# Kernel tuning notes

Hardware: AMD Instinct MI355X
Metric: run time of the kernel (lower is better)

Reference implementation:

```python
import jax, jax.numpy as jnp
import numpy as np

B, S, D, FF, E, TOP_K = 4, 2048, 1024, 4096, 8, 2


def setup_inputs() -> dict:
    key = jax.random.key(0)
    ks = jax.random.split(key, 13)
    sd = 1.0 / np.sqrt(D)
    sf = 1.0 / np.sqrt(FF)
    return {
        "x":   jax.random.normal(ks[0], (B, S, D), jnp.float32),
        # parallel 2-way router
        "Wr":  jax.random.normal(ks[1], (D, 2), jnp.float32) * sd,
        "br":  jnp.zeros((2,), jnp.float32),
        # MoE gate
        "Wg":  jax.random.normal(ks[2], (D, E), jnp.float32) * sd,
        "bg":  jnp.zeros((E,), jnp.float32),
        # expert FFNs
        "W1":  jax.random.normal(ks[3], (E, D, FF), jnp.float32) * sd,
        "b1":  jnp.zeros((E, FF), jnp.float32),
        "W2":  jax.random.normal(ks[4], (E, FF, D), jnp.float32) * sf,
        "b2":  jnp.zeros((E, D), jnp.float32),
        # dense FFN
        "D1":  jax.random.normal(ks[5], (D, FF), jnp.float32) * sd,
        "d1b": jnp.zeros((FF,), jnp.float32),
        "D2":  jax.random.normal(ks[6], (FF, D), jnp.float32) * sf,
        "d2b": jnp.zeros((D,), jnp.float32),
    }


def _hybrid_moe(x, Wr, br, Wg, bg, W1, b1, W2, b2, D1, d1b, D2, d2b):
    b, s, d = x.shape
    t = x.reshape(-1, d)                                  # [T, D]
    T = t.shape[0]

    # parallel 2-way blend router
    rp = jax.nn.softmax(x @ Wr + br, axis=-1)             # [B, S, 2]

    # MoE gating: softmax over experts, top-k, renormalize
    gp = jax.nn.softmax(t @ Wg + bg, axis=-1)             # [T, E]
    vals, idx = jax.lax.top_k(gp, TOP_K)                  # [T, K]
    vals = vals / jnp.sum(vals, axis=-1, keepdims=True)
    cw = jnp.zeros((T, E), t.dtype).at[jnp.arange(T)[:, None], idx].add(vals)  # [T, E]

    # expert FFNs (ReLU MLP), combined with top-k weights
    h = jax.nn.relu(jnp.einsum('td,edf->tef', t, W1) + b1)       # [T, E, FF]
    eo = jnp.einsum('tef,efd->ted', h, W2) + b2                  # [T, E, D]
    moe = jnp.einsum('te,ted->td', cw, eo).reshape(b, s, d)

    # dense FFN branch
    dense = jax.nn.relu(x @ D1 + d1b) @ D2 + d2b

    return rp[..., 0:1] * moe + rp[..., 1:2] * dense


def reference(x, Wr, br, Wg, bg, W1, b1, W2, b2, D1, d1b, D2, d2b):
    return _hybrid_moe(x, Wr, br, Wg, bg, W1, b1, W2, b2, D1, d1b, D2, d2b)
```

## Files before the change

kernel.cpp:

```cpp
#include <hip/hip_runtime.h>
#include <stdint.h>

#define T_TOK   8192
#define D_DIM   1024
#define FF_DIM  4096
#define E_NUM   8
#define SLOT_MAX 18432
#define RT_MAX  104

typedef unsigned int   u32;
typedef unsigned short u16;
typedef __attribute__((ext_vector_type(4))) float  f32x4;
typedef __attribute__((ext_vector_type(4))) float  f4;
typedef __attribute__((ext_vector_type(8))) short  bf16x8;
typedef __attribute__((ext_vector_type(8))) unsigned short u16x8;

__device__ __forceinline__ u16 f2bf(float f) {
  u32 u = __builtin_bit_cast(u32, f);
  return (u16)((u + 0x7fffu + ((u >> 16) & 1u)) >> 16);
}
__device__ __forceinline__ float bf2f(u16 h) {
  u32 u = ((u32)h) << 16; return __builtin_bit_cast(float, u);
}

typedef const __attribute__((address_space(1))) u32* gp1_t;
typedef __attribute__((address_space(3))) u32*       lp3_t;
__device__ __forceinline__ void gload16(const u16* g, u16* l) {
  __builtin_amdgcn_global_load_lds((gp1_t)(const void*)g, (lp3_t)l, 16, 0, 0);
}

__global__ void k_init(int* hdr) { if (threadIdx.x < 64) hdr[threadIdx.x] = 0; }

__global__ __launch_bounds__(256) void k_route(
    const float* __restrict__ x, const float* __restrict__ Wr, const float* __restrict__ br,
    const float* __restrict__ Wg, const float* __restrict__ bg,
    int* __restrict__ hdr, int4* __restrict__ tok_sel, float4* __restrict__ tok_wf,
    u16* __restrict__ xb)
{
  int w = threadIdx.x >> 6, l = threadIdx.x & 63;
  int t = blockIdx.x * 4 + w;
  const float* xt = x + (size_t)t * D_DIM;
  u16* xbt = xb + (size_t)t * D_DIM;
  float p[10];
  #pragma unroll
  for (int i = 0; i < 10; ++i) p[i] = 0.f;
  for (int j = 0; j < D_DIM / 64; ++j) {
    int d = j * 64 + l;
    float xv = xt[d];
    xbt[d] = f2bf(xv);
    p[0] += xv * Wr[d * 2 + 0];
    p[1] += xv * Wr[d * 2 + 1];
    f4 g0 = *(const f4*)&Wg[d * 8];
    f4 g1 = *(const f4*)&Wg[d * 8 + 4];
    p[2] += xv * g0[0]; p[3] += xv * g0[1]; p[4] += xv * g0[2]; p[5] += xv * g0[3];
    p[6] += xv * g1[0]; p[7] += xv * g1[1]; p[8] += xv * g1[2]; p[9] += xv * g1[3];
  }
  #pragma unroll
  for (int off = 32; off; off >>= 1) {
    #pragma unroll
    for (int i = 0; i < 10; ++i) p[i] += __shfl_xor(p[i], off, 64);
  }
  if (l == 0) {
    float a0 = p[0] + br[0], a1 = p[1] + br[1];
    float m  = fmaxf(a0, a1);
    float e0 = __expf(a0 - m), e1 = __expf(a1 - m);
    float rs = 1.f / (e0 + e1);
    float rp0 = e0 * rs, rp1 = e1 * rs;
    float g[E_NUM]; float gm = -1e30f;
    #pragma unroll
    for (int e = 0; e < E_NUM; ++e) { g[e] = p[2 + e] + bg[e]; gm = fmaxf(gm, g[e]); }
    int i0 = 0;
    #pragma unroll
    for (int e = 1; e < E_NUM; ++e) if (g[e] > g[i0]) i0 = e;
    int i1 = (i0 == 0) ? 1 : 0;
    #pragma unroll
    for (int e = 0; e < E_NUM; ++e) if (e != i0 && g[e] > g[i1]) i1 = e;
    float x0 = __expf(g[i0] - gm), x1 = __expf(g[i1] - gm);
    float s = 1.f / (x0 + x1);
    int r0 = atomicAdd(&hdr[i0], 1);
    int r1 = atomicAdd(&hdr[i1], 1);
    tok_sel[t] = make_int4(i0, r0, i1, r1);
    tok_wf[t]  = make_float4(x0 * s, x1 * s, rp0, rp1);
  }
}

__global__ __launch_bounds__(256) void k_offsets(int* __restrict__ hdr,
                                                 int4* __restrict__ tilemap,
                                                 int* __restrict__ perm)
{
  __shared__ int soff[E_NUM + 1];
  int tid = threadIdx.x;
  if (tid == 0) {
    int acc = 0;
    for (int e = 0; e < E_NUM; ++e) {
      soff[e] = acc; hdr[8 + e] = acc;
      acc += (hdr[e] + 255) & ~255;
    }
    soff[E_NUM] = acc;
    hdr[16] = acc;
    hdr[17] = acc >> 8;
    hdr[18] = (acc >> 8) + T_TOK / 256;
  }
  __syncthreads();
  int nmoe = soff[E_NUM] >> 8;
  for (int rt = tid; rt < RT_MAX; rt += 256) {
    int4 ent;
    if (rt < nmoe) {
      int row0 = rt * 256;
      int e = 0;
      while (e < E_NUM - 1 && row0 >= soff[e + 1]) ++e;
      ent = make_int4(0, row0, e, 0);
    } else if (rt < nmoe + T_TOK / 256) {
      ent = make_int4(1, (rt - nmoe) * 256, -1, 0);
    } else {
      ent = make_int4(-1, 0, 0, 0);
    }
    tilemap[rt] = ent;
  }
  for (int s = tid; s < SLOT_MAX; s += 256) perm[s] = -1;
}

__global__ void k_scatter(const int4* __restrict__ tok_sel, const int* __restrict__ hdr,
                          int* __restrict__ perm, int2* __restrict__ tok_slot)
{
  int t = blockIdx.x * 256 + threadIdx.x;
  if (t >= T_TOK) return;
  int4 s = tok_sel[t];
  int s0 = hdr[8 + s.x] + s.y;
  int s1 = hdr[8 + s.z] + s.w;
  perm[s0] = t; perm[s1] = t;
  tok_slot[t] = make_int2(s0, s1);
}

__global__ __launch_bounds__(256) void k_gather(const u16* __restrict__ xb,
                                                const int* __restrict__ perm,
                                                const int* __restrict__ hdr,
                                                u16* __restrict__ xg)
{
  int nslots = hdr[16];
  int row = blockIdx.x * 2 + (threadIdx.x >> 7);
  if (row >= nslots) return;
  int lane = threadIdx.x & 127;
  int t = perm[row];
  u16x8* dst = (u16x8*)(xg + (size_t)row * D_DIM) + lane;
  if (t < 0) { u16x8 z = {0,0,0,0,0,0,0,0}; *dst = z; }
  else       { *dst = *((const u16x8*)(xb + (size_t)t * D_DIM) + lane); }
}

__global__ __launch_bounds__(256) void k_tcast_all(
    const float* __restrict__ W1, const float* __restrict__ W2,
    const float* __restrict__ D1, const float* __restrict__ D2,
    u16* __restrict__ W1bt, u16* __restrict__ W2bt,
    u16* __restrict__ D1bt, u16* __restrict__ D2bt)
{
  int bid = blockIdx.x;
  int panel = bid >> 10, pb = bid & 1023;
  const float* s; u16* d; int R, C, ltc;
  if (panel < 8)       { s = W1 + (size_t)panel * D_DIM * FF_DIM; d = W1bt + (size_t)panel * D_DIM * FF_DIM; R = D_DIM;  C = FF_DIM; ltc = 6; }
  else if (panel < 16) { int e = panel - 8;
                         s = W2 + (size_t)e * FF_DIM * D_DIM;     d = W2bt + (size_t)e * FF_DIM * D_DIM;     R = FF_DIM; C = D_DIM;  ltc = 4; }
  else if (panel == 16){ s = D1; d = D1bt; R = D_DIM;  C = FF_DIM; ltc = 6; }
  else                 { s = D2; d = D2bt; R = FF_DIM; C = D_DIM;  ltc = 4; }
  int tc = pb & ((1 << ltc) - 1), tr = pb >> ltc;

  __shared__ float tile[64][65];
  int t = threadIdx.x;
  #pragma unroll
  for (int p = 0; p < 4; ++p) {
    int r = p * 16 + (t >> 4);
    int c4 = (t & 15) * 4;
    f4 v = *(const f4*)&s[(size_t)(tr * 64 + r) * C + tc * 64 + c4];
    tile[r][c4+0] = v[0]; tile[r][c4+1] = v[1]; tile[r][c4+2] = v[2]; tile[r][c4+3] = v[3];
  }
  __syncthreads();
  #pragma unroll
  for (int q = 0; q < 2; ++q) {
    int oc = q * 32 + (t >> 3);
    int r8 = (t & 7) * 8;
    u16x8 o;
    #pragma unroll
    for (int j = 0; j < 8; ++j) o[j] = f2bf(tile[r8 + j][oc]);
    *(u16x8*)&d[(size_t)(tc * 64 + oc) * R + tr * 64 + r8] = o;
  }
}

#define LGKM0() { asm volatile("s_waitcnt lgkmcnt(0)" ::: "memory"); \
                  __builtin_amdgcn_sched_barrier(0); }
#define BAR()   __builtin_amdgcn_s_barrier()

template <int RELU>
__global__ __launch_bounds__(512, 2) void k_gemm8p(
    const u16* __restrict__ Amoe, const u16* __restrict__ Aden,
    const u16* __restrict__ Bexp, const u16* __restrict__ Bden,
    const float* __restrict__ biasexp, const float* __restrict__ biasden,
    u16* __restrict__ Omoe, u16* __restrict__ Oden,
    const int* __restrict__ hdr, const int4* __restrict__ tilemap,
    int K, int N, long bexp_stride, int biasexp_stride, int lg2gx)
{
  int gx  = 1 << lg2gx;
  int nwg = gx * gridDim.y;
  int lin = blockIdx.y * gx + blockIdx.x;
  int sw  = (lin & 7) * (nwg >> 3) + (lin >> 3);
  int ct  = sw & (gx - 1);
  int rt  = sw >> lg2gx;
  if (rt >= hdr[18]) return;

  int4 ent = tilemap[rt];
  const u16* A; const u16* B; const float* bias; u16* O;
  if (ent.x == 1) { A = Aden; B = Bden; bias = biasden; O = Oden; }
  else {
    A = Amoe; B = Bexp + (size_t)ent.z * bexp_stride;
    bias = biasexp + (size_t)ent.z * biasexp_stride;
    O = Omoe;
  }
  const int row0 = ent.y;

  __shared__ __align__(16) u16 lds[65536];

  const int tid = threadIdx.x;
  const int wid = tid >> 6, l = tid & 63;
  const int wm = wid >> 2, wn = wid & 3;

  const int skel = ((l & 7) ^ (l >> 3)) * 8;
  const u16* aStage = A + (size_t)(row0     + wid * 8 + (l >> 3)) * K + skel;
  const u16* bStage = B + (size_t)(ct * 256 + wid * 8 + (l >> 3)) * K + skel;

  const int fr = l & 15, fq = l >> 4;
  const int fx = (l & 7) << 4;
  const int cs0 = (fq * 16) ^ fx;
  const int cs1 = (64 + fq * 16) ^ fx;
  const int brow = (wn & 1) * 64;
  const char* ldsc = (const char*)lds;
  const char* aP0 = ldsc + wm * 16384 + fr * 128 + cs0;
  const char* aP1 = ldsc + wm * 16384 + fr * 128 + cs1;
  const char* bP0 = ldsc + 65536 + (wn >> 1) * 16384 + (brow + fr) * 128 + cs0;
  const char* bP1 = ldsc + 65536 + (wn >> 1) * 16384 + (brow + fr) * 128 + cs1;

  auto STAGE_A = [&](int tt, int h, int bb) {
    const u16* src = aStage + (size_t)(h * 128) * K + (size_t)tt * 64;
    u16* dst = &lds[(bb * 2 + h) * 8192 + wid * 512];
    gload16(src, dst);
    gload16(src + (size_t)64 * K, dst + 4096);
  };
  auto STAGE_B = [&](int tt, int h, int bb) {
    const u16* src = bStage + (size_t)(h * 128) * K + (size_t)tt * 64;
    u16* dst = &lds[32768 + (bb * 2 + h) * 8192 + wid * 512];
    gload16(src, dst);
    gload16(src + (size_t)64 * K, dst + 4096);
  };

  f32x4 acc[8][4];
  #pragma unroll
  for (int m = 0; m < 8; ++m)
    #pragma unroll
    for (int n = 0; n < 4; ++n) acc[m][n] = (f32x4){0.f, 0.f, 0.f, 0.f};

  bf16x8 a0[4][2], a1[4][2], b0[2][2], b1[2][2];

  #define READ_A0(B_) { _Pragma("unroll") for (int j = 0; j < 4; ++j) { \
      a0[j][0] = *(const bf16x8*)(aP0 + ((B_)*32768 + j*2048)); \
      a0[j][1] = *(const bf16x8*)(aP1 + ((B_)*32768 + j*2048)); } }
  #define READ_A1(B_) { _Pragma("unroll") for (int j = 0; j < 4; ++j) { \
      a1[j][0] = *(const bf16x8*)(aP0 + ((B_)*32768 + 8192 + j*2048)); \
      a1[j][1] = *(const bf16x8*)(aP1 + ((B_)*32768 + 8192 + j*2048)); } }
  #define READ_B0(B_) { _Pragma("unroll") for (int i = 0; i < 2; ++i) { \
      b0[i][0] = *(const bf16x8*)(bP0 + ((B_)*32768 + i*2048)); \
      b0[i][1] = *(const bf16x8*)(bP1 + ((B_)*32768 + i*2048)); } }
  #define READ_B1(B_) { _Pragma("unroll") for (int i = 0; i < 2; ++i) { \
      b1[i][0] = *(const bf16x8*)(bP0 + ((B_)*32768 + 4096 + i*2048)); \
      b1[i][1] = *(const bf16x8*)(bP1 + ((B_)*32768 + 4096 + i*2048)); } }
  #define MFMA_Q(am, bm, mo, no) { __builtin_amdgcn_s_setprio(1); \
    _Pragma("unroll") for (int j = 0; j < 4; ++j) \
      _Pragma("unroll") for (int i = 0; i < 2; ++i) { \
        acc[(mo) + j][(no) + i] = __builtin_amdgcn_mfma_f32_16x16x32_bf16(am[j][0], bm[i][0], acc[(mo) + j][(no) + i], 0, 0, 0); \
        acc[(mo) + j][(no) + i] = __builtin_amdgcn_mfma_f32_16x16x32_bf16(am[j][1], bm[i][1], acc[(mo) + j][(no) + i], 0, 0, 0); } \
    __builtin_amdgcn_s_setprio(0); }

  const int NK = K >> 6;

  STAGE_B(0, 0, 0); STAGE_B(0, 1, 0); STAGE_A(0, 0, 0); STAGE_A(0, 1, 0);
  STAGE_B(1, 0, 1); STAGE_B(1, 1, 1); STAGE_A(1, 0, 1);
  asm volatile("s_waitcnt vmcnt(6)" ::: "memory");
  BAR();

  #define TILE(B_, t_) { \
     \
    READ_A0(B_); READ_B0(B_); \
    if ((t_) + 1 < NK) STAGE_A((t_) + 1, 1, (B_) ^ 1); \
    BAR(); LGKM0(); \
    MFMA_Q(a0, b0, 0, 0); \
    BAR(); \
     \
    READ_B1(B_); \
    BAR(); LGKM0(); \
    MFMA_Q(a0, b1, 0, 2); \
    BAR(); \
     \
    READ_A1(B_); \
    if ((t_) + 2 < NK) STAGE_B((t_) + 2, 0, (B_)); \
    BAR(); LGKM0(); \
    MFMA_Q(a1, b1, 4, 2); \
    BAR(); \
     \
    if ((t_) + 2 < NK) { STAGE_B((t_) + 2, 1, (B_)); STAGE_A((t_) + 2, 0, (B_)); } \
    BAR(); \
    MFMA_Q(a1, b0, 4, 0); \
    if ((t_) < NK - 2) { asm volatile("s_waitcnt vmcnt(6)" ::: "memory"); } \
    else               { asm volatile("s_waitcnt vmcnt(0)" ::: "memory"); } \
    BAR(); \
    __builtin_amdgcn_sched_barrier(0); }

  for (int t = 0; t < NK; t += 2) {
    TILE(0, t);
    TILE(1, t + 1);
  }
  #undef TILE

  __syncthreads();
  float bv[4];
  #pragma unroll
  for (int ni = 0; ni < 4; ++ni) bv[ni] = bias[ct * 256 + wn * 64 + ni * 16 + fr];
  float* ep = (float*)((char*)lds + wid * 4608);
  const int row16 = l >> 2, cg = l & 3;
  #pragma unroll
  for (int mi = 0; mi < 8; ++mi) {
    #pragma unroll
    for (int ni = 0; ni < 4; ++ni) {
      f32x4 v = acc[mi][ni];
      #pragma unroll
      for (int j = 0; j < 4; ++j) {
        float f = v[j] + bv[ni];
        if (RELU) f = fmaxf(f, 0.f);
        ep[(fq * 4 + j) * 68 + ni * 16 + fr] = f;
      }
    }
    #pragma unroll
    for (int p = 0; p < 2; ++p) {
      f4 r0 = *(f4*)&ep[row16 * 68 + (cg + p * 4) * 8];
      f4 r1 = *(f4*)&ep[row16 * 68 + (cg + p * 4) * 8 + 4];
      u16x8 o;
      o[0]=f2bf(r0[0]); o[1]=f2bf(r0[1]); o[2]=f2bf(r0[2]); o[3]=f2bf(r0[3]);
      o[4]=f2bf(r1[0]); o[5]=f2bf(r1[1]); o[6]=f2bf(r1[2]); o[7]=f2bf(r1[3]);
      int rr = row0 + wm * 128 + mi * 16 + row16;
      int cc = ct * 256 + wn * 64 + (cg + p * 4) * 8;
      *(u16x8*)&O[(size_t)rr * N + cc] = o;
    }
  }
  #undef READ_A0
  #undef READ_A1
  #undef READ_B0
  #undef READ_B1
  #undef MFMA_Q
}

__global__ __launch_bounds__(128) void k_combine(
    const u16* __restrict__ eo, const u16* __restrict__ dense_o,
    const float4* __restrict__ tok_wf, const int2* __restrict__ tok_slot,
    float* __restrict__ out)
{
  int t = blockIdx.x;
  int c8 = threadIdx.x;
  float4 wf = tok_wf[t];
  int2 sl = tok_slot[t];
  u16x8 a  = *((const u16x8*)(eo + (size_t)sl.x * D_DIM) + c8);
  u16x8 b  = *((const u16x8*)(eo + (size_t)sl.y * D_DIM) + c8);
  u16x8 dn = *((const u16x8*)(dense_o + (size_t)t * D_DIM) + c8);
  float* op = out + (size_t)t * D_DIM + c8 * 8;
  #pragma unroll
  for (int j = 0; j < 8; ++j) {
    float mo = wf.x * bf2f(a[j]) + wf.y * bf2f(b[j]);
    op[j] = wf.z * mo + wf.w * bf2f(dn[j]);
  }
}

extern "C" void kernel_launch(void* const* d_in, const int* in_sizes, int n_in,
                              void* d_out, int out_size, void* d_ws, size_t ws_size,
                              hipStream_t stream)
{
  const float* x   = (const float*)d_in[0];
  const float* Wr  = (const float*)d_in[1];
  const float* br  = (const float*)d_in[2];
  const float* Wg  = (const float*)d_in[3];
  const float* bg  = (const float*)d_in[4];
  const float* W1  = (const float*)d_in[5];
  const float* b1  = (const float*)d_in[6];
  const float* W2  = (const float*)d_in[7];
  const float* b2  = (const float*)d_in[8];
  const float* D1  = (const float*)d_in[9];
  const float* d1b = (const float*)d_in[10];
  const float* D2  = (const float*)d_in[11];
  const float* d2b = (const float*)d_in[12];
  float* out = (float*)d_out;

  char* base = (char*)d_ws;
  size_t cur = 0;
  auto alloc = [&](size_t b) -> void* {
    void* p = base + cur; cur = (cur + b + 255) & ~(size_t)255; return p;
  };
  int*    hdr      = (int*)   alloc(256 * sizeof(int));
  int4*   tilemap  = (int4*)  alloc((size_t)RT_MAX * sizeof(int4));
  int4*   tok_sel  = (int4*)  alloc((size_t)T_TOK * sizeof(int4));
  float4* tok_wf   = (float4*)alloc((size_t)T_TOK * sizeof(float4));
  int2*   tok_slot = (int2*)  alloc((size_t)T_TOK * sizeof(int2));
  int*    perm     = (int*)   alloc((size_t)SLOT_MAX * sizeof(int));
  u16*    xb       = (u16*)   alloc((size_t)T_TOK * D_DIM * 2);
  u16*    xg       = (u16*)   alloc((size_t)SLOT_MAX * D_DIM * 2);
  u16*    W1bt     = (u16*)   alloc((size_t)E_NUM * D_DIM * FF_DIM * 2);
  u16*    W2bt     = (u16*)   alloc((size_t)E_NUM * D_DIM * FF_DIM * 2);
  u16*    D1bt     = (u16*)   alloc((size_t)D_DIM * FF_DIM * 2);
  u16*    D2bt     = (u16*)   alloc((size_t)D_DIM * FF_DIM * 2);
  u16*    h_moe    = (u16*)   alloc((size_t)SLOT_MAX * FF_DIM * 2);
  u16*    h_dense  = (u16*)   alloc((size_t)T_TOK * FF_DIM * 2);
  u16*    eo       = (u16*)   alloc((size_t)SLOT_MAX * D_DIM * 2);
  u16*    dense_o  = (u16*)   alloc((size_t)T_TOK * D_DIM * 2);
  (void)in_sizes; (void)n_in; (void)out_size; (void)ws_size;

  k_init     <<<1, 64, 0, stream>>>(hdr);
  k_route    <<<T_TOK / 4, 256, 0, stream>>>(x, Wr, br, Wg, bg, hdr, tok_sel, tok_wf, xb);
  k_offsets  <<<1, 256, 0, stream>>>(hdr, tilemap, perm);
  k_scatter  <<<T_TOK / 256, 256, 0, stream>>>(tok_sel, hdr, perm, tok_slot);
  k_gather   <<<SLOT_MAX / 2, 256, 0, stream>>>(xb, perm, hdr, xg);
  k_tcast_all<<<18 * 1024, 256, 0, stream>>>(W1, W2, D1, D2, W1bt, W2bt, D1bt, D2bt);

  k_gemm8p<1><<<dim3(FF_DIM / 256, RT_MAX), 512, 0, stream>>>(
      xg, xb, W1bt, D1bt, b1, d1b, h_moe, h_dense, hdr, tilemap,
      D_DIM, FF_DIM, (long)D_DIM * FF_DIM, FF_DIM, 4);
  k_gemm8p<0><<<dim3(D_DIM / 256, RT_MAX), 512, 0, stream>>>(
      h_moe, h_dense, W2bt, D2bt, b2, d2b, eo, dense_o, hdr, tilemap,
      FF_DIM, D_DIM, (long)D_DIM * FF_DIM, D_DIM, 2);

  k_combine<<<T_TOK, 128, 0, stream>>>(eo, dense_o, tok_wf, tok_slot, out);
}
```

Before: 775.3 us.

## Fuse token gather into first GEMM's A-loads and merge setup kernels

Removes the separate gather kernel and xg buffer: the first grouped GEMM now reads A rows straight from the bf16 token buffer through per-row pointers taken from the perm table, so the extra write and read of the gathered activations goes away. The offset and scatter kernels are merged into one single-block setup kernel, and the init kernel becomes a memset. The routing kernel now loads x, Wr and Wg as 4-wide vectors. In exchange, the single-block setup loops over all 8192 tokens serially, and GEMM A-staging uses per-row indirect addresses, which costs more registers.

```diff
diff --git a/kernel.cpp b/kernel.cpp
--- a/kernel.cpp
+++ b/kernel.cpp
@@ -14,6 +14,7 @@
 typedef __attribute__((ext_vector_type(4))) float  f4;
 typedef __attribute__((ext_vector_type(8))) short  bf16x8;
 typedef __attribute__((ext_vector_type(8))) unsigned short u16x8;
+typedef __attribute__((ext_vector_type(4))) unsigned short u16x4;
 
 __device__ __forceinline__ u16 f2bf(float f) {
   u32 u = __builtin_bit_cast(u32, f);
@@ -28,8 +29,6 @@
 __device__ __forceinline__ void gload16(const u16* g, u16* l) {
   __builtin_amdgcn_global_load_lds((gp1_t)(const void*)g, (lp3_t)l, 16, 0, 0);
 }
-
-__global__ void k_init(int* hdr) { if (threadIdx.x < 64) hdr[threadIdx.x] = 0; }
 
 __global__ __launch_bounds__(256) void k_route(
     const float* __restrict__ x, const float* __restrict__ Wr, const float* __restrict__ br,
@@ -44,16 +43,23 @@
   float p[10];
   #pragma unroll
   for (int i = 0; i < 10; ++i) p[i] = 0.f;
-  for (int j = 0; j < D_DIM / 64; ++j) {
-    int d = j * 64 + l;
-    float xv = xt[d];
-    xbt[d] = f2bf(xv);
-    p[0] += xv * Wr[d * 2 + 0];
-    p[1] += xv * Wr[d * 2 + 1];
-    f4 g0 = *(const f4*)&Wg[d * 8];
-    f4 g1 = *(const f4*)&Wg[d * 8 + 4];
-    p[2] += xv * g0[0]; p[3] += xv * g0[1]; p[4] += xv * g0[2]; p[5] += xv * g0[3];
-    p[6] += xv * g1[0]; p[7] += xv * g1[1]; p[8] += xv * g1[2]; p[9] += xv * g1[3];
+  #pragma unroll
+  for (int j = 0; j < 4; ++j) {
+    int d0 = j * 256 + l * 4;
+    f4 xv = *(const f4*)&xt[d0];
+    u16x4 xo; xo[0]=f2bf(xv[0]); xo[1]=f2bf(xv[1]); xo[2]=f2bf(xv[2]); xo[3]=f2bf(xv[3]);
+    *(u16x4*)&xbt[d0] = xo;
+    f4 wra = *(const f4*)&Wr[d0 * 2];
+    f4 wrb = *(const f4*)&Wr[d0 * 2 + 4];
+    p[0] += xv[0]*wra[0] + xv[1]*wra[2] + xv[2]*wrb[0] + xv[3]*wrb[2];
+    p[1] += xv[0]*wra[1] + xv[1]*wra[3] + xv[2]*wrb[1] + xv[3]*wrb[3];
+    #pragma unroll
+    for (int i = 0; i < 4; ++i) {
+      f4 g0 = *(const f4*)&Wg[(size_t)(d0 + i) * 8];
+      f4 g1 = *(const f4*)&Wg[(size_t)(d0 + i) * 8 + 4];
+      p[2] += xv[i]*g0[0]; p[3] += xv[i]*g0[1]; p[4] += xv[i]*g0[2]; p[5] += xv[i]*g0[3];
+      p[6] += xv[i]*g1[0]; p[7] += xv[i]*g1[1]; p[8] += xv[i]*g1[2]; p[9] += xv[i]*g1[3];
+    }
   }
   #pragma unroll
   for (int off = 32; off; off >>= 1) {
@@ -84,9 +90,9 @@
   }
 }
 
-__global__ __launch_bounds__(256) void k_offsets(int* __restrict__ hdr,
-                                                 int4* __restrict__ tilemap,
-                                                 int* __restrict__ perm)
+__global__ __launch_bounds__(256) void k_setup(
+    int* __restrict__ hdr, int4* __restrict__ tilemap, int* __restrict__ perm,
+    const int4* __restrict__ tok_sel, int2* __restrict__ tok_slot)
 {
   __shared__ int soff[E_NUM + 1];
   int tid = threadIdx.x;
@@ -118,33 +124,14 @@
     tilemap[rt] = ent;
   }
   for (int s = tid; s < SLOT_MAX; s += 256) perm[s] = -1;
-}
-
-__global__ void k_scatter(const int4* __restrict__ tok_sel, const int* __restrict__ hdr,
-                          int* __restrict__ perm, int2* __restrict__ tok_slot)
-{
-  int t = blockIdx.x * 256 + threadIdx.x;
-  if (t >= T_TOK) return;
-  int4 s = tok_sel[t];
-  int s0 = hdr[8 + s.x] + s.y;
-  int s1 = hdr[8 + s.z] + s.w;
-  perm[s0] = t; perm[s1] = t;
-  tok_slot[t] = make_int2(s0, s1);
-}
-
-__global__ __launch_bounds__(256) void k_gather(const u16* __restrict__ xb,
-                                                const int* __restrict__ perm,
-                                                const int* __restrict__ hdr,
-                                                u16* __restrict__ xg)
-{
-  int nslots = hdr[16];
-  int row = blockIdx.x * 2 + (threadIdx.x >> 7);
-  if (row >= nslots) return;
-  int lane = threadIdx.x & 127;
-  int t = perm[row];
-  u16x8* dst = (u16x8*)(xg + (size_t)row * D_DIM) + lane;
-  if (t < 0) { u16x8 z = {0,0,0,0,0,0,0,0}; *dst = z; }
-  else       { *dst = *((const u16x8*)(xb + (size_t)t * D_DIM) + lane); }
+  __syncthreads();
+  for (int t = tid; t < T_TOK; t += 256) {
+    int4 s = tok_sel[t];
+    int s0 = soff[s.x] + s.y;
+    int s1 = soff[s.z] + s.w;
+    perm[s0] = t; perm[s1] = t;
+    tok_slot[t] = make_int2(s0, s1);
+  }
 }
 
 __global__ __launch_bounds__(256) void k_tcast_all(
@@ -188,13 +175,14 @@
                   __builtin_amdgcn_sched_barrier(0); }
 #define BAR()   __builtin_amdgcn_s_barrier()
 
-template <int RELU>
+template <int RELU, int GATHER>
 __global__ __launch_bounds__(512, 2) void k_gemm8p(
     const u16* __restrict__ Amoe, const u16* __restrict__ Aden,
     const u16* __restrict__ Bexp, const u16* __restrict__ Bden,
     const float* __restrict__ biasexp, const float* __restrict__ biasden,
     u16* __restrict__ Omoe, u16* __restrict__ Oden,
     const int* __restrict__ hdr, const int4* __restrict__ tilemap,
+    const int* __restrict__ perm,
     int K, int N, long bexp_stride, int biasexp_stride, int lg2gx)
 {
   int gx  = 1 << lg2gx;
@@ -206,10 +194,10 @@
   if (rt >= hdr[18]) return;
 
   int4 ent = tilemap[rt];
-  const u16* A; const u16* B; const float* bias; u16* O;
-  if (ent.x == 1) { A = Aden; B = Bden; bias = biasden; O = Oden; }
+  const u16* B; const float* bias; u16* O;
+  if (ent.x == 1) { B = Bden; bias = biasden; O = Oden; }
   else {
-    A = Amoe; B = Bexp + (size_t)ent.z * bexp_stride;
+    B = Bexp + (size_t)ent.z * bexp_stride;
     bias = biasexp + (size_t)ent.z * biasexp_stride;
     O = Omoe;
   }
@@ -221,9 +209,20 @@
   const int wid = tid >> 6, l = tid & 63;
   const int wm = wid >> 2, wn = wid & 3;
 
+  const int srow = wid * 8 + (l >> 3);
   const int skel = ((l & 7) ^ (l >> 3)) * 8;
-  const u16* aStage = A + (size_t)(row0     + wid * 8 + (l >> 3)) * K + skel;
-  const u16* bStage = B + (size_t)(ct * 256 + wid * 8 + (l >> 3)) * K + skel;
+  const u16* aSrcP[4];
+  const u16* bSrcP[4];
+  #pragma unroll
+  for (int i = 0; i < 4; ++i) {
+    int r = srow + i * 64;
+    if (ent.x == 1)      aSrcP[i] = Aden + (size_t)(row0 + r) * K + skel;
+    else if (GATHER) {
+      int pr = perm[row0 + r]; pr = pr < 0 ? 0 : pr;
+      aSrcP[i] = Amoe + (size_t)pr * K + skel;
+    } else               aSrcP[i] = Amoe + (size_t)(row0 + r) * K + skel;
+    bSrcP[i] = B + (size_t)(ct * 256 + r) * K + skel;
+  }
 
   const int fr = l & 15, fq = l >> 4;
   const int fx = (l & 7) << 4;
@@ -237,16 +236,14 @@
   const char* bP1 = ldsc + 65536 + (wn >> 1) * 16384 + (brow + fr) * 128 + cs1;
 
   auto STAGE_A = [&](int tt, int h, int bb) {
-    const u16* src = aStage + (size_t)(h * 128) * K + (size_t)tt * 64;
     u16* dst = &lds[(bb * 2 + h) * 8192 + wid * 512];
-    gload16(src, dst);
-    gload16(src + (size_t)64 * K, dst + 4096);
+    gload16(aSrcP[h * 2]     + tt * 64, dst);
+    gload16(aSrcP[h * 2 + 1] + tt * 64, dst + 4096);
   };
   auto STAGE_B = [&](int tt, int h, int bb) {
-    const u16* src = bStage + (size_t)(h * 128) * K + (size_t)tt * 64;
     u16* dst = &lds[32768 + (bb * 2 + h) * 8192 + wid * 512];
-    gload16(src, dst);
-    gload16(src + (size_t)64 * K, dst + 4096);
+    gload16(bSrcP[h * 2]     + tt * 64, dst);
+    gload16(bSrcP[h * 2 + 1] + tt * 64, dst + 4096);
   };
 
   f32x4 acc[8][4];
@@ -404,7 +401,6 @@
   int2*   tok_slot = (int2*)  alloc((size_t)T_TOK * sizeof(int2));
   int*    perm     = (int*)   alloc((size_t)SLOT_MAX * sizeof(int));
   u16*    xb       = (u16*)   alloc((size_t)T_TOK * D_DIM * 2);
-  u16*    xg       = (u16*)   alloc((size_t)SLOT_MAX * D_DIM * 2);
   u16*    W1bt     = (u16*)   alloc((size_t)E_NUM * D_DIM * FF_DIM * 2);
   u16*    W2bt     = (u16*)   alloc((size_t)E_NUM * D_DIM * FF_DIM * 2);
   u16*    D1bt     = (u16*)   alloc((size_t)D_DIM * FF_DIM * 2);
@@ -415,18 +411,16 @@
   u16*    dense_o  = (u16*)   alloc((size_t)T_TOK * D_DIM * 2);
   (void)in_sizes; (void)n_in; (void)out_size; (void)ws_size;
 
-  k_init     <<<1, 64, 0, stream>>>(hdr);
+  hipMemsetAsync(hdr, 0, 256 * sizeof(int), stream);
   k_route    <<<T_TOK / 4, 256, 0, stream>>>(x, Wr, br, Wg, bg, hdr, tok_sel, tok_wf, xb);
-  k_offsets  <<<1, 256, 0, stream>>>(hdr, tilemap, perm);
-  k_scatter  <<<T_TOK / 256, 256, 0, stream>>>(tok_sel, hdr, perm, tok_slot);
-  k_gather   <<<SLOT_MAX / 2, 256, 0, stream>>>(xb, perm, hdr, xg);
+  k_setup    <<<1, 256, 0, stream>>>(hdr, tilemap, perm, tok_sel, tok_slot);
   k_tcast_all<<<18 * 1024, 256, 0, stream>>>(W1, W2, D1, D2, W1bt, W2bt, D1bt, D2bt);
 
-  k_gemm8p<1><<<dim3(FF_DIM / 256, RT_MAX), 512, 0, stream>>>(
-      xg, xb, W1bt, D1bt, b1, d1b, h_moe, h_dense, hdr, tilemap,
+  k_gemm8p<1, 1><<<dim3(FF_DIM / 256, RT_MAX), 512, 0, stream>>>(
+      xb, xb, W1bt, D1bt, b1, d1b, h_moe, h_dense, hdr, tilemap, perm,
       D_DIM, FF_DIM, (long)D_DIM * FF_DIM, FF_DIM, 4);
-  k_gemm8p<0><<<dim3(D_DIM / 256, RT_MAX), 512, 0, stream>>>(
-      h_moe, h_dense, W2bt, D2bt, b2, d2b, eo, dense_o, hdr, tilemap,
+  k_gemm8p<0, 0><<<dim3(D_DIM / 256, RT_MAX), 512, 0, stream>>>(
+      h_moe, h_dense, W2bt, D2bt, b2, d2b, eo, dense_o, hdr, tilemap, perm,
       FF_DIM, D_DIM, (long)D_DIM * FF_DIM, D_DIM, 2);
 
   k_combine<<<T_TOK, 128, 0, stream>>>(eo, dense_o, tok_wf, tok_slot, out);
```

Result: no change. 780.5 us (+0.7%).
